# Optimization experiments

Hardware: AMD Instinct MI355X
Metric: run time of the kernel (lower is better)

Reference implementation:

```python
import jax, jax.numpy as jnp
import numpy as np

L = 16384   # nodes (rows)
E = 131072  # edges
SP = 20000  # column positions (nodes + periodic images)
C = 512     # embed_dim
H = 8       # heads
DH = C // H # head dim = 64
HID = 1024  # ffn hidden


def setup_inputs() -> dict:
    key = jax.random.key(0)
    ks = jax.random.split(key, 16)
    p = lambda k, shape: jax.random.normal(k, shape, dtype=jnp.float32) * 0.02
    return dict(
        x=jax.random.normal(ks[0], (L, C), dtype=jnp.float32),
        row_index=jax.random.randint(ks[1], (E,), 0, L),
        col_index=jax.random.randint(ks[2], (E,), 0, L),
        to_col_index=jax.random.randint(ks[3], (E,), 0, SP),
        att_bias=jax.random.normal(ks[4], (E, H), dtype=jnp.float32),
        pos_att_bias=jax.random.normal(ks[5], (E, H), dtype=jnp.float32),
        dist=jax.random.uniform(ks[6], (E,), minval=0.5, maxval=5.0),
        pos=jax.random.normal(ks[7], (L, 3), dtype=jnp.float32),
        col_pos=jax.random.normal(ks[8], (SP, 3), dtype=jnp.float32),
        ln1_g=jnp.ones((C,), jnp.float32), ln1_b=jnp.zeros((C,), jnp.float32),
        ln2_g=jnp.ones((C,), jnp.float32), ln2_b=jnp.zeros((C,), jnp.float32),
        Wq=p(ks[9], (C, C)), bq=jnp.zeros((C,), jnp.float32),
        Wk=p(ks[10], (C, C)), bk=jnp.zeros((C,), jnp.float32),
        Wv=p(ks[11], (C, C)), bv=jnp.zeros((C,), jnp.float32),
        Wvec=p(ks[12], (3, C)), bvec=jnp.zeros((C,), jnp.float32),
        Wo=p(ks[13], (C, C)), bo=jnp.zeros((C,), jnp.float32),
        W1=p(ks[14], (C, HID)), b1=jnp.zeros((HID,), jnp.float32),
        W2=p(ks[15], (HID, C)), b2=jnp.zeros((C,), jnp.float32),
    )


def _ln(x, g, b, eps=1e-5):
    mu = jnp.mean(x, -1, keepdims=True)
    v = jnp.mean((x - mu) ** 2, -1, keepdims=True)
    return (x - mu) * jax.lax.rsqrt(v + eps) * g + b


def reference(x, row_index, col_index, to_col_index, att_bias, pos_att_bias,
              dist, pos, col_pos, ln1_g, ln1_b, ln2_g, ln2_b,
              Wq, bq, Wk, bk, Wv, bv, Wvec, bvec, Wo, bo, W1, b1, W2, b2):
    Lx = x.shape[0]
    # --- pre-norm + Euclidean sparse attention ---
    z = _ln(x, ln1_g, ln1_b)
    q = (z @ Wq + bq).reshape(Lx, H, DH)
    k = (z @ Wk + bk).reshape(Lx, H, DH)
    v = (z @ Wv + bv).reshape(Lx, H, DH)
    qe = q[row_index]          # (E,H,DH) gather
    ke = k[col_index]          # (E,H,DH)
    ve = v[col_index]          # (E,H,DH)
    # relative unit direction from receiving node to (PBC-shifted) column node
    rel = (col_pos[to_col_index] - pos[row_index]) / dist[:, None]   # (E,3)
    ve = ve + (rel @ Wvec + bvec).reshape(-1, H, DH)
    # Euclidean (negative squared L2) attention score + positional bias
    score = -jnp.sum((qe - ke) ** 2, axis=-1) / np.float32(np.sqrt(DH)) + pos_att_bias  # (E,H)
    # segment softmax over edges grouped by row_index
    m = jax.ops.segment_max(score, row_index, num_segments=Lx)       # (L,H)
    m = jnp.where(jnp.isfinite(m), m, 0.0)
    pexp = jnp.exp(score - m[row_index])
    den = jax.ops.segment_sum(pexp, row_index, num_segments=Lx)      # (L,H)
    deng = den[row_index]
    alpha = pexp / jnp.where(deng == 0.0, 1.0, deng)                 # (E,H)
    out = jax.ops.segment_sum(alpha[:, :, None] * ve, row_index, num_segments=Lx)
    att = out.reshape(Lx, C) @ Wo + bo
    x = x + att
    # --- pre-norm + feed-forward ---
    z2 = _ln(x, ln2_g, ln2_b)
    ff = jax.nn.gelu(z2 @ W1 + b1) @ W2 + b2
    return x + ff
```

## Files before the change

kernel.cpp:

```cpp
#include <hip/hip_runtime.h>

#define L_NODES 16384
#define E_EDGES 131072
#define CDIM 512
#define QKVDIM 1536
#define HEADS 8
#define DHEAD 64
#define HID 1024

typedef __attribute__((ext_vector_type(8))) short bf16x8;
typedef __attribute__((ext_vector_type(4))) float f32x4;

__device__ inline unsigned short f2b(float f) {
    union { float f; unsigned int u; } v{f};
    unsigned int r = (v.u + 0x7fffu + ((v.u >> 16) & 1u)) >> 16;
    return (unsigned short)r;
}
__device__ inline float b2f(unsigned short h) {
    union { unsigned int u; float f; } v;
    v.u = (unsigned int)h << 16;
    return v.f;
}

__device__ inline void async_lds16(const void* g, void* l) {
    __builtin_amdgcn_global_load_lds(
        (const __attribute__((address_space(1))) unsigned int*)g,
        (__attribute__((address_space(3))) unsigned int*)l,
        16, 0, 0);
}

__global__ __launch_bounds__(256) void ln_bf16_kernel(
    const float* __restrict__ x, const float* __restrict__ g,
    const float* __restrict__ b, short* __restrict__ out)
{
    int row = blockIdx.x;
    int t = threadIdx.x;
    const float2* xr = (const float2*)(x + (size_t)row * CDIM);
    float2 v = xr[t];
    float s = v.x + v.y;
    float sq = v.x * v.x + v.y * v.y;
    for (int off = 32; off; off >>= 1) {
        s += __shfl_xor(s, off);
        sq += __shfl_xor(sq, off);
    }
    __shared__ float ss[4], sqs[4];
    int wave = t >> 6, lane = t & 63;
    if (lane == 0) { ss[wave] = s; sqs[wave] = sq; }
    __syncthreads();
    s = ss[0] + ss[1] + ss[2] + ss[3];
    sq = sqs[0] + sqs[1] + sqs[2] + sqs[3];
    float mu = s * (1.0f / CDIM);
    float var = sq * (1.0f / CDIM) - mu * mu;
    float inv = rsqrtf(var + 1e-5f);
    int c = t * 2;
    unsigned short h0 = f2b((v.x - mu) * inv * g[c] + b[c]);
    unsigned short h1 = f2b((v.y - mu) * inv * g[c + 1] + b[c + 1]);
    unsigned int packed = ((unsigned int)h1 << 16) | h0;
    *(unsigned int*)(out + (size_t)row * CDIM + c) = packed;
}

__global__ __launch_bounds__(256) void prep_kernel(
    const float* __restrict__ Wq, const float* __restrict__ Wk,
    const float* __restrict__ Wv, const float* __restrict__ Wo,
    const float* __restrict__ W1, const float* __restrict__ W2,
    short* __restrict__ wqkvT, short* __restrict__ woT,
    short* __restrict__ w1T, short* __restrict__ w2T,
    const float* __restrict__ bq, const float* __restrict__ bk,
    const float* __restrict__ bv, float* __restrict__ bqkv,
    int* __restrict__ cnt)
{
    int bid = blockIdx.x;
    if (bid >= 2054) {
        cnt[(bid - 2054) * 256 + threadIdx.x] = 0;
        return;
    }
    if (bid >= 2048) {
        int i = (bid - 2048) * 256 + threadIdx.x;
        float val = (i < CDIM) ? bq[i] : (i < 2 * CDIM) ? bk[i - CDIM] : bv[i - 2 * CDIM];
        bqkv[i] = val;
        return;
    }
    const float* W; short* WT; int K, N, tn, tk;
    if (bid < 1024) {
        int w = bid >> 8, local = bid & 255;
        tn = local & 15; tk = local >> 4; K = 512; N = 512;
        W = (w == 0) ? Wq : (w == 1) ? Wk : (w == 2) ? Wv : Wo;
        WT = (w == 3) ? woT : wqkvT + (size_t)w * 512 * 512;
    } else if (bid < 1536) {
        int local = bid - 1024;
        tn = local & 31; tk = local >> 5; K = 512; N = 1024;
        W = W1; WT = w1T;
    } else {
        int local = bid - 1536;
        tn = local & 15; tk = local >> 4; K = 1024; N = 512;
        W = W2; WT = w2T;
    }
    __shared__ float tile[32][33];
    int tx = threadIdx.x & 31, ty = threadIdx.x >> 5;
    int n0 = tn * 32, k0 = tk * 32;
#pragma unroll
    for (int r = 0; r < 4; r++)
        tile[ty + r * 8][tx] = W[(size_t)(k0 + ty + r * 8) * N + n0 + tx];
    __syncthreads();
#pragma unroll
    for (int r = 0; r < 4; r++)
        WT[(size_t)(n0 + ty + r * 8) * K + k0 + tx] = f2b(tile[tx][ty + r * 8]);
}

__global__ __launch_bounds__(256) void gemm_bf16_kernel(
    const short* __restrict__ A, const short* __restrict__ B,
    const float* __restrict__ bias, const float* __restrict__ res,
    float* __restrict__ outf, short* __restrict__ outb,
    int M, int N, int K, int act)
{
    __shared__ short As[128 * 32];
    __shared__ short Bs[128 * 32];
    int t = threadIdx.x;
    int bm = blockIdx.y * 128, bn = blockIdx.x * 128;
    int wave = t >> 6, lane = t & 63;
    int wm = (wave & 1) * 64, wn = (wave >> 1) * 64;
    int crow = lane & 15, quad = lane >> 4;

    f32x4 acc[4][4] = {};

    for (int k0 = 0; k0 < K; k0 += 32) {
#pragma unroll
        for (int c = 0; c < 2; c++) {
            int idx = c * 256 + t;
            int row = idx >> 2, chunk = idx & 3;
            async_lds16(A + (size_t)(bm + row) * K + k0 + chunk * 8,
                        (char*)As + c * 4096 + wave * 1024 + lane * 16);
            async_lds16(B + (size_t)(bn + row) * K + k0 + chunk * 8,
                        (char*)Bs + c * 4096 + wave * 1024 + lane * 16);
        }
        __syncthreads();
        bf16x8 af[4], bg[4];
#pragma unroll
        for (int i = 0; i < 4; i++)
            af[i] = *(const bf16x8*)&As[(wm + i * 16 + crow) * 32 + quad * 8];
#pragma unroll
        for (int j = 0; j < 4; j++)
            bg[j] = *(const bf16x8*)&Bs[(wn + j * 16 + crow) * 32 + quad * 8];
#pragma unroll
        for (int i = 0; i < 4; i++)
#pragma unroll
            for (int j = 0; j < 4; j++)
                acc[i][j] = __builtin_amdgcn_mfma_f32_16x16x32_bf16(af[i], bg[j], acc[i][j], 0, 0, 0);
        __syncthreads();
    }

#pragma unroll
    for (int i = 0; i < 4; i++) {
#pragma unroll
        for (int j = 0; j < 4; j++) {
            int n = bn + wn + j * 16 + crow;
            float bi = bias ? bias[n] : 0.0f;
#pragma unroll
            for (int r = 0; r < 4; r++) {
                int mrow = bm + wm + i * 16 + quad * 4 + r;
                float val = acc[i][j][r] + bi;
                if (act) {
                    float u = 0.7978845608028654f * (val + 0.044715f * val * val * val);
                    val = 0.5f * val * (1.0f + tanhf(u));
                }
                if (res) val += res[(size_t)mrow * N + n];
                if (outf) outf[(size_t)mrow * N + n] = val;
                if (outb) outb[(size_t)mrow * N + n] = f2b(val);
            }
        }
    }
}

__global__ void hist_kernel(const int* __restrict__ row_index, int* __restrict__ cnt)
{
    int e = blockIdx.x * 256 + threadIdx.x;
    if (e < E_EDGES) atomicAdd(&cnt[row_index[e]], 1);
}

__global__ void scan_kernel(const int* __restrict__ cnt, int* __restrict__ row_start,
                            int* __restrict__ cursor)
{
    int t = threadIdx.x;
    const int PER = L_NODES / 64;
    int local = 0;
    for (int i = 0; i < PER; i++) local += cnt[t * PER + i];
    int v = local;
    for (int off = 1; off < 64; off <<= 1) {
        int u = __shfl_up(v, off);
        if (t >= off) v += u;
    }
    int run = v - local;
    for (int i = 0; i < PER; i++) {
        row_start[t * PER + i] = run;
        cursor[t * PER + i] = run;
        run += cnt[t * PER + i];
    }
    if (t == 63) row_start[L_NODES] = run;
}

__global__ void scatter_kernel(const int* __restrict__ row_index, const int* __restrict__ col_index,
                               const int* __restrict__ to_col_index, const float* __restrict__ dist,
                               const float* __restrict__ pos, const float* __restrict__ col_pos,
                               const float* __restrict__ pos_att_bias,
                               int* __restrict__ cursor, int4* __restrict__ emeta,
                               float* __restrict__ pabp)
{
    int e = blockIdx.x * 256 + threadIdx.x;
    if (e < E_EDGES) {
        int row = row_index[e];
        int p = atomicAdd(&cursor[row], 1);
        int tci = to_col_index[e];
        float dinv = 1.0f / dist[e];
        float r0 = (col_pos[tci * 3]     - pos[row * 3])     * dinv;
        float r1 = (col_pos[tci * 3 + 1] - pos[row * 3 + 1]) * dinv;
        float r2 = (col_pos[tci * 3 + 2] - pos[row * 3 + 2]) * dinv;
        emeta[p] = make_int4(col_index[e], __float_as_int(r0), __float_as_int(r1),
                             __float_as_int(r2));
        const float4* pb = (const float4*)(pos_att_bias + (size_t)e * HEADS);
        float4 b0 = pb[0], b1 = pb[1];
        float4* dst = (float4*)(pabp + (size_t)p * HEADS);
        dst[0] = b0; dst[1] = b1;
    }
}

__global__ __launch_bounds__(256) void attn_kernel(
    const short* __restrict__ qkv, const int4* __restrict__ emeta,
    const float* __restrict__ pabp, const int* __restrict__ row_start,
    const float* __restrict__ Wvec, const float* __restrict__ bvec,
    short* __restrict__ out_bf)
{
    int lane = threadIdx.x & 63;
    int r = blockIdx.x * 4 + (threadIdx.x >> 6);
    int h = lane >> 3;
    int cbase = lane * 8;

    float qv[8], wv0[8], wv1[8], wv2[8], bvv[8];
    {
        bf16x8 qh = *(const bf16x8*)(qkv + (size_t)r * QKVDIM + cbase);
#pragma unroll
        for (int j = 0; j < 8; j++) qv[j] = b2f((unsigned short)qh[j]);
        float4 a0 = *(const float4*)(Wvec + cbase);
        float4 a1 = *(const float4*)(Wvec + cbase + 4);
        float4 b0 = *(const float4*)(Wvec + CDIM + cbase);
        float4 b1 = *(const float4*)(Wvec + CDIM + cbase + 4);
        float4 c0 = *(const float4*)(Wvec + 2 * CDIM + cbase);
        float4 c1 = *(const float4*)(Wvec + 2 * CDIM + cbase + 4);
        float4 d0 = *(const float4*)(bvec + cbase);
        float4 d1 = *(const float4*)(bvec + cbase + 4);
        wv0[0]=a0.x; wv0[1]=a0.y; wv0[2]=a0.z; wv0[3]=a0.w; wv0[4]=a1.x; wv0[5]=a1.y; wv0[6]=a1.z; wv0[7]=a1.w;
        wv1[0]=b0.x; wv1[1]=b0.y; wv1[2]=b0.z; wv1[3]=b0.w; wv1[4]=b1.x; wv1[5]=b1.y; wv1[6]=b1.z; wv1[7]=b1.w;
        wv2[0]=c0.x; wv2[1]=c0.y; wv2[2]=c0.z; wv2[3]=c0.w; wv2[4]=c1.x; wv2[5]=c1.y; wv2[6]=c1.z; wv2[7]=c1.w;
        bvv[0]=d0.x; bvv[1]=d0.y; bvv[2]=d0.z; bvv[3]=d0.w; bvv[4]=d1.x; bvv[5]=d1.y; bvv[6]=d1.z; bvv[7]=d1.w;
    }

    int e0 = row_start[r], e1 = row_start[r + 1];
    float m = -1e30f, l = 0.0f;
    float acc[8] = {};

    int4 em_n, em_n2;
    float pab_n;
    bf16x8 k_n, v_n;
    if (e0 < e1) {
        em_n = emeta[e0];
        em_n2 = emeta[(e0 + 1 < e1) ? e0 + 1 : e1 - 1];
        pab_n = pabp[(size_t)e0 * HEADS + h];
        const short* kp = qkv + (size_t)em_n.x * QKVDIM + CDIM + cbase;
        k_n = *(const bf16x8*)kp;
        v_n = *(const bf16x8*)(kp + CDIM);
    }
    for (int idx = e0; idx < e1; ++idx) {
        int4 em = em_n;
        float pab = pab_n;
        bf16x8 k8 = k_n, v8 = v_n;
        em_n = em_n2;
        int i2 = (idx + 2 < e1) ? idx + 2 : e1 - 1;
        em_n2 = emeta[i2];
        int i1 = (idx + 1 < e1) ? idx + 1 : e1 - 1;
        pab_n = pabp[(size_t)i1 * HEADS + h];
        {
            const short* kp = qkv + (size_t)em_n.x * QKVDIM + CDIM + cbase;
            k_n = *(const bf16x8*)kp;
            v_n = *(const bf16x8*)(kp + CDIM);
        }
        float s = 0.0f;
        float vf[8];
#pragma unroll
        for (int j = 0; j < 8; j++) {
            float kf = b2f((unsigned short)k8[j]);
            vf[j] = b2f((unsigned short)v8[j]);
            float d = qv[j] - kf;
            s = fmaf(d, d, s);
        }
        s += __shfl_xor(s, 1);
        s += __shfl_xor(s, 2);
        s += __shfl_xor(s, 4);
        float score = -s * 0.125f + pab;
        float mn = fmaxf(m, score);
        float scale = __expf(m - mn);
        float pexp = __expf(score - mn);
        m = mn;
        l = l * scale + pexp;
        float r0 = __int_as_float(em.y), r1 = __int_as_float(em.z), r2 = __int_as_float(em.w);
#pragma unroll
        for (int j = 0; j < 8; j++) {
            float vv = vf[j] + r0 * wv0[j] + r1 * wv1[j] + r2 * wv2[j] + bvv[j];
            acc[j] = fmaf(acc[j], scale, pexp * vv);
        }
    }
    float inv = (l > 0.0f) ? 1.0f / l : 0.0f;
    bf16x8 o;
#pragma unroll
    for (int j = 0; j < 8; j++) o[j] = (short)f2b(acc[j] * inv);
    *(bf16x8*)(out_bf + (size_t)r * CDIM + cbase) = o;
}

extern "C" void kernel_launch(void* const* d_in, const int* in_sizes, int n_in,
                              void* d_out, int out_size, void* d_ws, size_t ws_size,
                              hipStream_t stream)
{
    const float* x            = (const float*)d_in[0];
    const int*   row_index    = (const int*)d_in[1];
    const int*   col_index    = (const int*)d_in[2];
    const int*   to_col_index = (const int*)d_in[3];
    const float* pos_att_bias = (const float*)d_in[5];
    const float* dist         = (const float*)d_in[6];
    const float* pos          = (const float*)d_in[7];
    const float* col_pos      = (const float*)d_in[8];
    const float* ln1_g = (const float*)d_in[9];
    const float* ln1_b = (const float*)d_in[10];
    const float* ln2_g = (const float*)d_in[11];
    const float* ln2_b = (const float*)d_in[12];
    const float* Wq = (const float*)d_in[13];  const float* bq = (const float*)d_in[14];
    const float* Wk = (const float*)d_in[15];  const float* bk = (const float*)d_in[16];
    const float* Wv = (const float*)d_in[17];  const float* bv = (const float*)d_in[18];
    const float* Wvec = (const float*)d_in[19]; const float* bvec = (const float*)d_in[20];
    const float* Wo = (const float*)d_in[21];  const float* bo = (const float*)d_in[22];
    const float* W1 = (const float*)d_in[23];  const float* b1 = (const float*)d_in[24];
    const float* W2 = (const float*)d_in[25];  const float* b2 = (const float*)d_in[26];

    char* ws = (char*)d_ws;
    size_t off = 0;
    auto alloc = [&](size_t bytes) -> void* {
        void* p = ws + off;
        off = (off + bytes + 255) & ~(size_t)255;
        return p;
    };
    const size_t LC = (size_t)L_NODES * CDIM;
    short* qkvb = (short*)alloc((size_t)L_NODES * QKVDIM * 2);
    float* x1f  = (float*)alloc(LC * 4);
    short* zbf  = (short*)alloc(LC * 2);
    short* abf  = (short*)alloc(LC * 2);
    short* wqkvT = (short*)alloc((size_t)QKVDIM * CDIM * 2);
    short* woT   = (short*)alloc((size_t)CDIM * CDIM * 2);
    short* w1T   = (short*)alloc((size_t)CDIM * HID * 2);
    short* w2T   = (short*)alloc((size_t)HID * CDIM * 2);
    float* bqkv  = (float*)alloc(QKVDIM * 4);
    int* cnt       = (int*)alloc(L_NODES * 4);
    int* cursor    = (int*)alloc(L_NODES * 4);
    int* row_start = (int*)alloc((L_NODES + 1) * 4);
    int4* emeta    = (int4*)alloc((size_t)E_EDGES * 16);
    short* hbf = (short*)qkvb;
    float* pabp = x1f;

    prep_kernel<<<2118, 256, 0, stream>>>(Wq, Wk, Wv, Wo, W1, W2,
                                          wqkvT, woT, w1T, w2T,
                                          bq, bk, bv, bqkv, cnt);

    ln_bf16_kernel<<<L_NODES, 256, 0, stream>>>(x, ln1_g, ln1_b, zbf);

    dim3 gqkv(QKVDIM / 128, L_NODES / 128);
    gemm_bf16_kernel<<<gqkv, 256, 0, stream>>>(zbf, wqkvT, bqkv, nullptr, nullptr, qkvb,
                                               L_NODES, QKVDIM, CDIM, 0);

    hist_kernel<<<E_EDGES / 256, 256, 0, stream>>>(row_index, cnt);
    scan_kernel<<<1, 64, 0, stream>>>(cnt, row_start, cursor);
    scatter_kernel<<<E_EDGES / 256, 256, 0, stream>>>(row_index, col_index, to_col_index,
                                                      dist, pos, col_pos, pos_att_bias,
                                                      cursor, emeta, pabp);

    attn_kernel<<<L_NODES / 4, 256, 0, stream>>>(qkvb, emeta, pabp, row_start, Wvec, bvec, abf);

    dim3 g512(CDIM / 128, L_NODES / 128);
    gemm_bf16_kernel<<<g512, 256, 0, stream>>>(abf, woT, bo, x, x1f, nullptr, L_NODES, CDIM, CDIM, 0);

    ln_bf16_kernel<<<L_NODES, 256, 0, stream>>>(x1f, ln2_g, ln2_b, zbf);

    dim3 g1024(HID / 128, L_NODES / 128);
    gemm_bf16_kernel<<<g1024, 256, 0, stream>>>(zbf, w1T, b1, nullptr, nullptr, hbf, L_NODES, HID, CDIM, 1);
    gemm_bf16_kernel<<<g512, 256, 0, stream>>>(hbf, w2T, b2, x1f, (float*)d_out, nullptr, L_NODES, CDIM, HID, 0);
}
```

Baseline: 442.3 us.

## Double-buffer GEMM LDS tiles and use exp-based GELU

```diff
diff --git a/kernel.cpp b/kernel.cpp
--- a/kernel.cpp
+++ b/kernel.cpp
@@ -113,8 +113,8 @@
     float* __restrict__ outf, short* __restrict__ outb,
     int M, int N, int K, int act)
 {
-    __shared__ short As[128 * 32];
-    __shared__ short Bs[128 * 32];
+    __shared__ short As[2][128 * 32];
+    __shared__ short Bs[2][128 * 32];
     int t = threadIdx.x;
     int bm = blockIdx.y * 128, bn = blockIdx.x * 128;
     int wave = t >> 6, lane = t & 63;
@@ -123,30 +123,48 @@
 
     f32x4 acc[4][4] = {};
 
-    for (int k0 = 0; k0 < K; k0 += 32) {
-#pragma unroll
-        for (int c = 0; c < 2; c++) {
-            int idx = c * 256 + t;
-            int row = idx >> 2, chunk = idx & 3;
-            async_lds16(A + (size_t)(bm + row) * K + k0 + chunk * 8,
-                        (char*)As + c * 4096 + wave * 1024 + lane * 16);
-            async_lds16(B + (size_t)(bn + row) * K + k0 + chunk * 8,
-                        (char*)Bs + c * 4096 + wave * 1024 + lane * 16);
+    const int niter = K >> 5;
+#pragma unroll
+    for (int c = 0; c < 2; c++) {
+        int idx = c * 256 + t;
+        int row = idx >> 2, chunk = idx & 3;
+        async_lds16(A + (size_t)(bm + row) * K + chunk * 8,
+                    (char*)As + c * 4096 + wave * 1024 + lane * 16);
+        async_lds16(B + (size_t)(bn + row) * K + chunk * 8,
+                    (char*)Bs + c * 4096 + wave * 1024 + lane * 16);
+    }
+
+    for (int i = 0; i < niter; ++i) {
+        int cur = i & 1;
+        asm volatile("s_waitcnt vmcnt(0)" ::: "memory");
+        __builtin_amdgcn_s_barrier();
+        if (i + 1 < niter) {
+            int k0 = (i + 1) << 5;
+            int nxt = cur ^ 1;
+#pragma unroll
+            for (int c = 0; c < 2; c++) {
+                int idx = c * 256 + t;
+                int row = idx >> 2, chunk = idx & 3;
+                async_lds16(A + (size_t)(bm + row) * K + k0 + chunk * 8,
+                            (char*)As + nxt * 8192 + c * 4096 + wave * 1024 + lane * 16);
+                async_lds16(B + (size_t)(bn + row) * K + k0 + chunk * 8,
+                            (char*)Bs + nxt * 8192 + c * 4096 + wave * 1024 + lane * 16);
+            }
         }
-        __syncthreads();
+        const short* Ab = (const short*)((const char*)As + cur * 8192);
+        const short* Bb = (const short*)((const char*)Bs + cur * 8192);
         bf16x8 af[4], bg[4];
 #pragma unroll
-        for (int i = 0; i < 4; i++)
-            af[i] = *(const bf16x8*)&As[(wm + i * 16 + crow) * 32 + quad * 8];
+        for (int ii = 0; ii < 4; ii++)
+            af[ii] = *(const bf16x8*)&Ab[(wm + ii * 16 + crow) * 32 + quad * 8];
 #pragma unroll
         for (int j = 0; j < 4; j++)
-            bg[j] = *(const bf16x8*)&Bs[(wn + j * 16 + crow) * 32 + quad * 8];
-#pragma unroll
-        for (int i = 0; i < 4; i++)
+            bg[j] = *(const bf16x8*)&Bb[(wn + j * 16 + crow) * 32 + quad * 8];
+#pragma unroll
+        for (int ii = 0; ii < 4; ii++)
 #pragma unroll
             for (int j = 0; j < 4; j++)
-                acc[i][j] = __builtin_amdgcn_mfma_f32_16x16x32_bf16(af[i], bg[j], acc[i][j], 0, 0, 0);
-        __syncthreads();
+                acc[ii][j] = __builtin_amdgcn_mfma_f32_16x16x32_bf16(af[ii], bg[j], acc[ii][j], 0, 0, 0);
     }
 
 #pragma unroll
@@ -160,8 +178,8 @@
                 int mrow = bm + wm + i * 16 + quad * 4 + r;
                 float val = acc[i][j][r] + bi;
                 if (act) {
-                    float u = 0.7978845608028654f * (val + 0.044715f * val * val * val);
-                    val = 0.5f * val * (1.0f + tanhf(u));
+                    float u = 1.5957691216057308f * (val + 0.044715f * val * val * val);
+                    val = val / (1.0f + __expf(-u));
                 }
                 if (res) val += res[(size_t)mrow * N + n];
                 if (outf) outf[(size_t)mrow * N + n] = val;
```

Measured after the change: 427.4 us. 3.4% less time.
